# Performance work log

Hardware: AMD Instinct MI355X
Metric: run time of the kernel (lower is better)

## Reference

```python
import jax, jax.numpy as jnp
import numpy as np

EMBED_DIM = 1024
NUM_HEADS = 16
HEAD_DIM = EMBED_DIM // NUM_HEADS
B, T = 4, 2048


def setup_inputs() -> dict:
    key = jax.random.key(0)
    ks = jax.random.split(key, 5)
    s = 1.0 / np.sqrt(EMBED_DIM)
    x = jax.random.normal(ks[0], (B, T, EMBED_DIM), dtype=jnp.float32)
    attention_mask = jnp.ones((B, 1, 1, T), dtype=jnp.int32)
    # torch Linear weights: qkv (3E, E), out (E, E); store transposed for x @ W
    W_qkv = jax.random.uniform(ks[1], (EMBED_DIM, 3 * EMBED_DIM), jnp.float32, -s, s)
    b_qkv = jax.random.uniform(ks[2], (3 * EMBED_DIM,), jnp.float32, -s, s)
    W_out = jax.random.uniform(ks[3], (EMBED_DIM, EMBED_DIM), jnp.float32, -s, s)
    b_out = jax.random.uniform(ks[4], (EMBED_DIM,), jnp.float32, -s, s)
    return {"x": x, "attention_mask": attention_mask,
            "W_qkv": W_qkv, "b_qkv": b_qkv, "W_out": W_out, "b_out": b_out}


def reference(x, attention_mask, W_qkv, b_qkv, W_out, b_out):
    Bq, Tq, E = x.shape
    qkv = x @ W_qkv + b_qkv                              # [B,T,3E]
    qkv = qkv.reshape(Bq, Tq, 3, NUM_HEADS, HEAD_DIM)
    qkv = jnp.transpose(qkv, (2, 0, 3, 1, 4))            # [3,B,H,T,d]
    q, k, v = qkv[0], qkv[1], qkv[2]
    scores = jnp.einsum('bhqd,bhkd->bhqk', q, k) / jnp.sqrt(
        jnp.asarray(HEAD_DIM, x.dtype))                  # [B,H,T,T]
    scores = jnp.where(attention_mask == 0, jnp.asarray(-jnp.inf, x.dtype), scores)
    attn = jax.nn.softmax(scores, axis=-1)
    ctx = jnp.einsum('bhqk,bhkd->bhqd', attn, v)         # [B,H,T,d]
    ctx = jnp.transpose(ctx, (0, 2, 1, 3)).reshape(Bq, Tq, E)
    return ctx @ W_out + b_out
```

## Files before the change

kernel.cpp:

```cpp
#include <hip/hip_runtime.h>
#include <hip/hip_bf16.h>
#include <stdint.h>


typedef __attribute__((ext_vector_type(8))) short short8;
typedef __attribute__((ext_vector_type(4))) float f32x4;
typedef __attribute__((ext_vector_type(16))) float f32x16;
typedef __attribute__((ext_vector_type(4))) unsigned short ushort4_t;
typedef __attribute__((ext_vector_type(8))) unsigned short ushort8_t;

#define SEQ 2048
#define EDIM 1024
#define QSCALE 0.18033688011112042f

__device__ __forceinline__ unsigned short f2bf(float x) {
  union { float f; uint32_t u; } v; v.f = x;
  uint32_t r = v.u + 0x7fffu + ((v.u >> 16) & 1u);
  return (unsigned short)(r >> 16);
}

__device__ __forceinline__ uint32_t cvtpk(float lo, float hi) {
  uint32_t r;
  asm("v_cvt_pk_bf16_f32 %0, %1, %2" : "=v"(r) : "v"(lo), "v"(hi));
  return r;
}

__device__ __forceinline__ float exp2_raw(float x) {
  float r;
  asm("v_exp_f32 %0, %1" : "=v"(r) : "v"(x));
  return r;
}

__device__ __forceinline__ void gload_lds16(const void* g, void* l) {
  typedef __attribute__((address_space(1))) const unsigned int gu32;
  typedef __attribute__((address_space(3))) unsigned int lu32;
  __builtin_amdgcn_global_load_lds((gu32*)g, (lu32*)l, 16, 0, 0);
}

__global__ void k_prep(const float* __restrict__ x,
                       unsigned short* __restrict__ xb,
                       const float* __restrict__ Wq,
                       unsigned short* __restrict__ wqt,
                       const float* __restrict__ Wo,
                       unsigned short* __restrict__ wot) {
  __shared__ float tile[32][33];
  const int id = blockIdx.x;
  if (id < 4096) {
    const int i = id * 256 + threadIdx.x;
    const float4* p = ((const float4*)x) + (size_t)i * 2;
    float4 a = p[0], b = p[1];
    ushort8_t v;
    v[0] = f2bf(a.x); v[1] = f2bf(a.y); v[2] = f2bf(a.z); v[3] = f2bf(a.w);
    v[4] = f2bf(b.x); v[5] = f2bf(b.y); v[6] = f2bf(b.z); v[7] = f2bf(b.w);
    ((ushort8_t*)xb)[i] = v;
    return;
  }
  const float* W;
  unsigned short* Wt;
  int N, bx, by;
  if (id < 7168) { W = Wq; Wt = wqt; N = 3072; bx = (id - 4096) % 96; by = (id - 4096) / 96; }
  else           { W = Wo; Wt = wot; N = 1024; bx = (id - 7168) % 32; by = (id - 7168) / 32; }
  const int K = 1024;
  const int c0 = bx * 32, r0 = by * 32;
  const int tx = threadIdx.x & 31, ty = threadIdx.x >> 5;
#pragma unroll
  for (int i = 0; i < 4; ++i) {
    int r = ty + i * 8;
    tile[r][tx] = W[(size_t)(r0 + r) * N + c0 + tx];
  }
  __syncthreads();
#pragma unroll
  for (int i = 0; i < 4; ++i) {
    int r = ty + i * 8;
    Wt[(size_t)(c0 + r) * K + r0 + tx] = f2bf(tile[tx][r]);
  }
}

template <int EPI, int NBX>
__global__ __launch_bounds__(256, 2) void k_gemm(
    const unsigned short* __restrict__ A, const unsigned short* __restrict__ Bt,
    const float* __restrict__ bias, unsigned short* __restrict__ Qo,
    unsigned short* __restrict__ Ko, unsigned short* __restrict__ VTo,
    float* __restrict__ Out) {
  __shared__ unsigned short As[2][2][128 * 32];
  __shared__ unsigned short Bs[2][2][128 * 32];
  const int tid = threadIdx.x;
  const int lane = tid & 63, wid = tid >> 6;
  const int wr = wid >> 1, wc = wid & 1;
  const int g = lane >> 4, r = lane & 15;
  const int lid = blockIdx.y * NBX + blockIdx.x;
  const int total = NBX * gridDim.y;
  const int id = (lid & 7) * (total >> 3) + (lid >> 3);
  const int m0 = (id / NBX) * 128, n0 = (id % NBX) * 128;

  const int row0 = tid >> 2, sl0 = tid & 3;
  const unsigned short* a0 = A + (size_t)(m0 + row0) * 1024 + sl0 * 8;
  const unsigned short* a1 = A + (size_t)(m0 + 64 + row0) * 1024 + sl0 * 8;
  const unsigned short* b0 = Bt + (size_t)(n0 + row0) * 1024 + sl0 * 8;
  const unsigned short* b1 = Bt + (size_t)(n0 + 64 + row0) * 1024 + sl0 * 8;
  char* adst = (char*)As + wid * 64 * 16;
  char* bdst = (char*)Bs + wid * 64 * 16;

  auto STAGE = [&](int buf) {
    const int bo = buf * 16384;
    gload_lds16(a0,      adst + bo);
    gload_lds16(a1,      adst + bo + 4096);
    gload_lds16(a0 + 32, adst + bo + 8192);
    gload_lds16(a1 + 32, adst + bo + 8192 + 4096);
    gload_lds16(b0,      bdst + bo);
    gload_lds16(b1,      bdst + bo + 4096);
    gload_lds16(b0 + 32, bdst + bo + 8192);
    gload_lds16(b1 + 32, bdst + bo + 8192 + 4096);
    a0 += 64; a1 += 64; b0 += 64; b1 += 64;
  };

  f32x4 zero4 = {0.f, 0.f, 0.f, 0.f};
  f32x4 acc[4][4];
#pragma unroll
  for (int mi = 0; mi < 4; ++mi)
#pragma unroll
    for (int ni = 0; ni < 4; ++ni) acc[mi][ni] = zero4;

  STAGE(0);
  asm volatile("s_waitcnt vmcnt(0)" ::: "memory");
  __builtin_amdgcn_s_barrier();

  for (int t = 0; t < 16; ++t) {
    const int cur = t & 1;
    if (t < 15) STAGE(cur ^ 1);
#pragma unroll
    for (int sub = 0; sub < 2; ++sub) {
      short8 af[4], bf[4];
#pragma unroll
      for (int mi = 0; mi < 4; ++mi)
        af[mi] = *(const short8*)&As[cur][sub][(wr * 64 + mi * 16 + r) * 32 + g * 8];
#pragma unroll
      for (int ni = 0; ni < 4; ++ni)
        bf[ni] = *(const short8*)&Bs[cur][sub][(wc * 64 + ni * 16 + r) * 32 + g * 8];
#pragma unroll
      for (int mi = 0; mi < 4; ++mi)
#pragma unroll
        for (int ni = 0; ni < 4; ++ni)
          acc[mi][ni] = __builtin_amdgcn_mfma_f32_16x16x32_bf16(
              af[mi], bf[ni], acc[mi][ni], 0, 0, 0);
    }
    asm volatile("s_waitcnt vmcnt(0)" ::: "memory");
    __builtin_amdgcn_s_barrier();
  }

#pragma unroll
  for (int mi = 0; mi < 4; ++mi) {
#pragma unroll
    for (int ni = 0; ni < 4; ++ni) {
      const int n = n0 + wc * 64 + ni * 16 + r;
      const float bv = bias[n];
      const int mbase = m0 + wr * 64 + mi * 16 + g * 4;
      if (EPI == 0) {
        const int sec = n >> 10, e = n & 1023, h = e >> 6, dd = e & 63;
        const int b = mbase >> 11, t = mbase & 2047;
        if (sec == 2) {
          ushort4_t pk;
#pragma unroll
          for (int j = 0; j < 4; ++j) pk[j] = f2bf(acc[mi][ni][j] + bv);
          *(ushort4_t*)&VTo[(((size_t)b * 16 + h) * 64 + dd) * 2048 + t] = pk;
        } else {
          unsigned short* dst = (sec == 0) ? Qo : Ko;
          const float scl = (sec == 0) ? QSCALE : 1.0f;
#pragma unroll
          for (int j = 0; j < 4; ++j)
            dst[(((size_t)b * 16 + h) * 2048 + t + j) * 64 + dd] =
                f2bf((acc[mi][ni][j] + bv) * scl);
        }
      } else {
#pragma unroll
        for (int j = 0; j < 4; ++j)
          Out[(size_t)(mbase + j) * 1024 + n] = acc[mi][ni][j] + bv;
      }
    }
  }
}

__global__ __launch_bounds__(512, 4) void k_attn(
    const unsigned short* __restrict__ Qg, const unsigned short* __restrict__ Kg,
    const unsigned short* __restrict__ VTg, const int* __restrict__ maskp,
    unsigned short* __restrict__ ctx) {
  __shared__ unsigned short Ks[2][64 * 64];
  __shared__ unsigned short Vs[2][64 * 64];
  const int tid = threadIdx.x, lane = tid & 63, wid = tid >> 6;
  const int q = lane & 31, hi = lane >> 5;
  const int id = blockIdx.x;
  const int slot = id >> 3;
  const int bh = (id & 7) * 8 + (slot >> 3);
  const int b = bh >> 4, h = bh & 15;
  const int q0 = (slot & 7) * 256 + wid * 32;
  const int qr = q0 + q;

  const unsigned short* Qb = Qg + (size_t)bh * SEQ * 64;
  const unsigned short* Kb = Kg + (size_t)bh * SEQ * 64;
  const unsigned short* Vb = VTg + (size_t)bh * 64 * SEQ;
  const int* mb = maskp + b * SEQ;

  const int r0_ = tid >> 3, sl0_ = (tid & 7) ^ (r0_ & 7);
  const unsigned short* kp0 = Kb + r0_ * 64 + sl0_ * 8;
  const unsigned short* vp0 = Vb + (size_t)r0_ * SEQ + sl0_ * 8;
  char* kbase = (char*)Ks[0] + wid * 1024;
  char* vbase = (char*)Vs[0] + wid * 1024;

  auto STAGE = [&](int buf) {
    const int bo = buf * 8192;
    gload_lds16(kp0, kbase + bo);
    gload_lds16(vp0, vbase + bo);
    kp0 += 64 * 64;
    vp0 += 64;
  };

  short8 qf[4];
#pragma unroll
  for (int ds = 0; ds < 4; ++ds)
    qf[ds] = *(const short8*)&Qb[(size_t)qr * 64 + ds * 16 + hi * 8];

  short8 onesf;
#pragma unroll
  for (int j = 0; j < 8; ++j) onesf[j] = (short)0x3F80;

  f32x16 z16 = {0.f,0.f,0.f,0.f,0.f,0.f,0.f,0.f,0.f,0.f,0.f,0.f,0.f,0.f,0.f,0.f};
  f32x16 o0 = z16, o1 = z16;
  f32x16 osum = z16;
  const int kb4 = hi * 4;

  STAGE(0);
  const int* mptr = mb + lane;
  int mv = mptr[0];
  mptr += 64;

  for (int t = 0; t < 32; ++t) {
    const int cur = t & 1;
    __syncthreads();
    int mvn = 1;
    if (t < 31) {
      STAGE(cur ^ 1);
      mvn = mptr[0];
      mptr += 64;
    }
    const unsigned long long bits = __ballot(mv != 0);
    mv = mvn;

    const char* KsB = (const char*)Ks[cur];
    const char* VsB = (const char*)Vs[cur];
    f32x16 c0 = z16, c1 = z16;
    __builtin_amdgcn_s_setprio(1);
#pragma unroll
    for (int ds = 0; ds < 4; ++ds) {
      const int sl = ds * 2 + hi;
      short8 ka0 = *(const short8*)(KsB + q * 128 + ((sl ^ (q & 7)) * 16));
      short8 ka1 = *(const short8*)(KsB + (32 + q) * 128 + ((sl ^ (q & 7)) * 16));
      c0 = __builtin_amdgcn_mfma_f32_32x32x16_bf16(ka0, qf[ds], c0, 0, 0, 0);
      c1 = __builtin_amdgcn_mfma_f32_32x32x16_bf16(ka1, qf[ds], c1, 0, 0, 0);
    }
    __builtin_amdgcn_s_setprio(0);

#pragma unroll
    for (int i = 0; i < 16; ++i) {
      c0[i] = exp2_raw(c0[i]);
      c1[i] = exp2_raw(c1[i]);
    }
    if (bits != ~0ull) {
#pragma unroll
      for (int i = 0; i < 16; ++i) {
        const int k0 = (i & 3) + 8 * (i >> 2) + kb4;
        if (!((bits >> k0) & 1)) c0[i] = 0.f;
        if (!((bits >> (k0 + 32)) & 1)) c1[i] = 0.f;
      }
    }

    short8 pf[4];
#pragma unroll
    for (int sub = 0; sub < 2; ++sub) {
      uint32_t w[8];
#pragma unroll
      for (int j = 0; j < 8; ++j)
        w[j] = sub ? cvtpk(c1[2 * j], c1[2 * j + 1])
                   : cvtpk(c0[2 * j], c0[2 * j + 1]);
      asm("v_permlane32_swap_b32 %0, %1" : "+v"(w[0]), "+v"(w[2]));
      asm("v_permlane32_swap_b32 %0, %1" : "+v"(w[1]), "+v"(w[3]));
      asm("v_permlane32_swap_b32 %0, %1" : "+v"(w[4]), "+v"(w[6]));
      asm("v_permlane32_swap_b32 %0, %1" : "+v"(w[5]), "+v"(w[7]));
      union { uint32_t u[4]; short8 s; } ua, ub;
      ua.u[0] = w[0]; ua.u[1] = w[1]; ua.u[2] = w[2]; ua.u[3] = w[3];
      ub.u[0] = w[4]; ub.u[1] = w[5]; ub.u[2] = w[6]; ub.u[3] = w[7];
      pf[sub * 2] = ua.s;
      pf[sub * 2 + 1] = ub.s;
    }

    __builtin_amdgcn_s_setprio(1);
#pragma unroll
    for (int ks = 0; ks < 4; ++ks) {
      const int sl = ks * 2 + hi;
      short8 va0 = *(const short8*)(VsB + q * 128 + ((sl ^ (q & 7)) * 16));
      short8 va1 = *(const short8*)(VsB + (32 + q) * 128 + ((sl ^ (q & 7)) * 16));
      o0 = __builtin_amdgcn_mfma_f32_32x32x16_bf16(va0, pf[ks], o0, 0, 0, 0);
      o1 = __builtin_amdgcn_mfma_f32_32x32x16_bf16(va1, pf[ks], o1, 0, 0, 0);
      osum = __builtin_amdgcn_mfma_f32_32x32x16_bf16(onesf, pf[ks], osum,
                                                     0, 0, 0);
    }
    __builtin_amdgcn_s_setprio(0);
  }

  const float inv = 1.f / osum[0];
#pragma unroll
  for (int ns = 0; ns < 2; ++ns) {
#pragma unroll
    for (int g_ = 0; g_ < 4; ++g_) {
      ushort4_t v4;
#pragma unroll
      for (int e = 0; e < 4; ++e) {
        const float val = (ns ? o1[g_ * 4 + e] : o0[g_ * 4 + e]) * inv;
        v4[e] = f2bf(val);
      }
      *(ushort4_t*)&ctx[((size_t)b * SEQ + qr) * 1024 + h * 64 + ns * 32 +
                        g_ * 8 + hi * 4] = v4;
    }
  }
}

extern "C" void kernel_launch(void* const* d_in, const int* in_sizes, int n_in,
                              void* d_out, int out_size, void* d_ws,
                              size_t ws_size, hipStream_t stream) {
  const float* x = (const float*)d_in[0];
  const int* mask = (const int*)d_in[1];
  const float* Wqkv = (const float*)d_in[2];
  const float* bqkv = (const float*)d_in[3];
  const float* Wout = (const float*)d_in[4];
  const float* bout = (const float*)d_in[5];
  float* out = (float*)d_out;

  unsigned short* ws = (unsigned short*)d_ws;
  unsigned short* xb = ws;
  unsigned short* wqt = ws + 8388608;
  unsigned short* wot = ws + 11534336;
  unsigned short* Q = ws + 12582912;
  unsigned short* K = ws + 20971520;
  unsigned short* VT = ws + 29360128;
  unsigned short* ctx = xb;

  k_prep<<<8192, 256, 0, stream>>>(x, xb, Wqkv, wqt, Wout, wot);
  k_gemm<0, 24><<<dim3(24, 64), 256, 0, stream>>>(xb, wqt, bqkv, Q, K, VT,
                                                  nullptr);
  k_attn<<<512, 512, 0, stream>>>(Q, K, VT, mask, ctx);
  k_gemm<1, 8><<<dim3(8, 64), 256, 0, stream>>>(ctx, wot, bout, nullptr,
                                                nullptr, nullptr, out);
}
```

Before: 189.4 us.

## Load K/V fragments directly from global memory instead of staging through LDS

The attention kernel no longer double-buffers K and V tiles in shared memory with async global-to-LDS loads and per-iteration barriers. Each wave now reads its MFMA operand fragments straight from global memory, relying on L2 and L1 caching for reuse across the 8 waves in a block. This removes the __syncthreads and LDS traffic, but each wave issues redundant global loads and the prefetch overlap with compute is lost, so latency is exposed.

```diff
diff --git a/kernel.cpp b/kernel.cpp
--- a/kernel.cpp
+++ b/kernel.cpp
@@ -184,8 +184,6 @@
     const unsigned short* __restrict__ Qg, const unsigned short* __restrict__ Kg,
     const unsigned short* __restrict__ VTg, const int* __restrict__ maskp,
     unsigned short* __restrict__ ctx) {
-  __shared__ unsigned short Ks[2][64 * 64];
-  __shared__ unsigned short Vs[2][64 * 64];
   const int tid = threadIdx.x, lane = tid & 63, wid = tid >> 6;
   const int q = lane & 31, hi = lane >> 5;
   const int id = blockIdx.x;
@@ -200,24 +198,15 @@
   const unsigned short* Vb = VTg + (size_t)bh * 64 * SEQ;
   const int* mb = maskp + b * SEQ;
 
-  const int r0_ = tid >> 3, sl0_ = (tid & 7) ^ (r0_ & 7);
-  const unsigned short* kp0 = Kb + r0_ * 64 + sl0_ * 8;
-  const unsigned short* vp0 = Vb + (size_t)r0_ * SEQ + sl0_ * 8;
-  char* kbase = (char*)Ks[0] + wid * 1024;
-  char* vbase = (char*)Vs[0] + wid * 1024;
-
-  auto STAGE = [&](int buf) {
-    const int bo = buf * 8192;
-    gload_lds16(kp0, kbase + bo);
-    gload_lds16(vp0, vbase + bo);
-    kp0 += 64 * 64;
-    vp0 += 64;
-  };
-
   short8 qf[4];
 #pragma unroll
   for (int ds = 0; ds < 4; ++ds)
     qf[ds] = *(const short8*)&Qb[(size_t)qr * 64 + ds * 16 + hi * 8];
+
+  const unsigned short* kp0 = Kb + q * 64 + hi * 8;
+  const unsigned short* kp1 = Kb + (32 + q) * 64 + hi * 8;
+  const unsigned short* vp0 = Vb + (size_t)q * SEQ + hi * 8;
+  const unsigned short* vp1 = Vb + (size_t)(32 + q) * SEQ + hi * 8;
 
   short8 onesf;
 #pragma unroll
@@ -228,32 +217,15 @@
   f32x16 osum = z16;
   const int kb4 = hi * 4;
 
-  STAGE(0);
-  const int* mptr = mb + lane;
-  int mv = mptr[0];
-  mptr += 64;
-
   for (int t = 0; t < 32; ++t) {
-    const int cur = t & 1;
-    __syncthreads();
-    int mvn = 1;
-    if (t < 31) {
-      STAGE(cur ^ 1);
-      mvn = mptr[0];
-      mptr += 64;
-    }
-    const unsigned long long bits = __ballot(mv != 0);
-    mv = mvn;
-
-    const char* KsB = (const char*)Ks[cur];
-    const char* VsB = (const char*)Vs[cur];
+    const unsigned long long bits = __ballot(mb[t * 64 + lane] != 0);
+
     f32x16 c0 = z16, c1 = z16;
     __builtin_amdgcn_s_setprio(1);
 #pragma unroll
     for (int ds = 0; ds < 4; ++ds) {
-      const int sl = ds * 2 + hi;
-      short8 ka0 = *(const short8*)(KsB + q * 128 + ((sl ^ (q & 7)) * 16));
-      short8 ka1 = *(const short8*)(KsB + (32 + q) * 128 + ((sl ^ (q & 7)) * 16));
+      short8 ka0 = *(const short8*)(kp0 + ds * 16);
+      short8 ka1 = *(const short8*)(kp1 + ds * 16);
       c0 = __builtin_amdgcn_mfma_f32_32x32x16_bf16(ka0, qf[ds], c0, 0, 0, 0);
       c1 = __builtin_amdgcn_mfma_f32_32x32x16_bf16(ka1, qf[ds], c1, 0, 0, 0);
     }
@@ -295,15 +267,17 @@
     __builtin_amdgcn_s_setprio(1);
 #pragma unroll
     for (int ks = 0; ks < 4; ++ks) {
-      const int sl = ks * 2 + hi;
-      short8 va0 = *(const short8*)(VsB + q * 128 + ((sl ^ (q & 7)) * 16));
-      short8 va1 = *(const short8*)(VsB + (32 + q) * 128 + ((sl ^ (q & 7)) * 16));
+      short8 va0 = *(const short8*)(vp0 + ks * 16);
+      short8 va1 = *(const short8*)(vp1 + ks * 16);
       o0 = __builtin_amdgcn_mfma_f32_32x32x16_bf16(va0, pf[ks], o0, 0, 0, 0);
       o1 = __builtin_amdgcn_mfma_f32_32x32x16_bf16(va1, pf[ks], o1, 0, 0, 0);
       osum = __builtin_amdgcn_mfma_f32_32x32x16_bf16(onesf, pf[ks], osum,
                                                      0, 0, 0);
     }
     __builtin_amdgcn_s_setprio(0);
+
+    kp0 += 64 * 64; kp1 += 64 * 64;
+    vp0 += 64; vp1 += 64;
   }
 
   const float inv = 1.f / osum[0];
```

Result: slower. 341.9 us (+80.5%).

## Store GEMM and attention LDS tiles in MFMA fragment order for linear reads

Applied to the files above, without the earlier changes.

Reorganizes the shared-memory layout in both the projection GEMM and attention kernels so that global-to-LDS loads scatter data directly into per-lane MFMA fragment order. Each lane then reads its operand with a single contiguous lane*16 offset. This removes the XOR swizzle and row/column address arithmetic and avoids bank conflicts on ds_read. The cost is less coalesced global loads, since each lane now fetches 16-byte chunks from scattered rows.

```diff
diff --git a/kernel.cpp b/kernel.cpp
--- a/kernel.cpp
+++ b/kernel.cpp
@@ -82,8 +82,8 @@
     const float* __restrict__ bias, unsigned short* __restrict__ Qo,
     unsigned short* __restrict__ Ko, unsigned short* __restrict__ VTo,
     float* __restrict__ Out) {
-  __shared__ unsigned short As[2][2][128 * 32];
-  __shared__ unsigned short Bs[2][2][128 * 32];
+  __shared__ unsigned short As[2 * 8192];
+  __shared__ unsigned short Bs[2 * 8192];
   const int tid = threadIdx.x;
   const int lane = tid & 63, wid = tid >> 6;
   const int wr = wid >> 1, wc = wid & 1;
@@ -93,25 +93,29 @@
   const int id = (lid & 7) * (total >> 3) + (lid >> 3);
   const int m0 = (id / NBX) * 128, n0 = (id % NBX) * 128;
 
-  const int row0 = tid >> 2, sl0 = tid & 3;
-  const unsigned short* a0 = A + (size_t)(m0 + row0) * 1024 + sl0 * 8;
-  const unsigned short* a1 = A + (size_t)(m0 + 64 + row0) * 1024 + sl0 * 8;
-  const unsigned short* b0 = Bt + (size_t)(n0 + row0) * 1024 + sl0 * 8;
-  const unsigned short* b1 = Bt + (size_t)(n0 + 64 + row0) * 1024 + sl0 * 8;
-  char* adst = (char*)As + wid * 64 * 16;
-  char* bdst = (char*)Bs + wid * 64 * 16;
+  const unsigned short* ap[4];
+  const unsigned short* bp[4];
+#pragma unroll
+  for (int i = 0; i < 4; ++i) {
+    const int slot = i * 256 + tid;
+    const int sub = slot >> 9, mi = (slot >> 7) & 3, wrr = (slot >> 6) & 1;
+    const int l = slot & 63;
+    const int row = wrr * 64 + mi * 16 + (l & 15);
+    const int dof = sub * 32 + (l >> 4) * 8;
+    ap[i] = A + (size_t)(m0 + row) * 1024 + dof;
+    bp[i] = Bt + (size_t)(n0 + row) * 1024 + dof;
+  }
+  char* adst = (char*)As + wid * 1024;
+  char* bdst = (char*)Bs + wid * 1024;
 
   auto STAGE = [&](int buf) {
     const int bo = buf * 16384;
-    gload_lds16(a0,      adst + bo);
-    gload_lds16(a1,      adst + bo + 4096);
-    gload_lds16(a0 + 32, adst + bo + 8192);
-    gload_lds16(a1 + 32, adst + bo + 8192 + 4096);
-    gload_lds16(b0,      bdst + bo);
-    gload_lds16(b1,      bdst + bo + 4096);
-    gload_lds16(b0 + 32, bdst + bo + 8192);
-    gload_lds16(b1 + 32, bdst + bo + 8192 + 4096);
-    a0 += 64; a1 += 64; b0 += 64; b1 += 64;
+#pragma unroll
+    for (int i = 0; i < 4; ++i) {
+      gload_lds16(ap[i], adst + bo + i * 4096);
+      gload_lds16(bp[i], bdst + bo + i * 4096);
+      ap[i] += 64; bp[i] += 64;
+    }
   };
 
   f32x4 zero4 = {0.f, 0.f, 0.f, 0.f};
@@ -120,6 +124,10 @@
   for (int mi = 0; mi < 4; ++mi)
 #pragma unroll
     for (int ni = 0; ni < 4; ++ni) acc[mi][ni] = zero4;
+
+  const int myoff = lane * 16;
+  const char* abase = (const char*)As + wr * 1024 + myoff;
+  const char* bbase = (const char*)Bs + wc * 1024 + myoff;
 
   STAGE(0);
   asm volatile("s_waitcnt vmcnt(0)" ::: "memory");
@@ -128,15 +136,16 @@
   for (int t = 0; t < 16; ++t) {
     const int cur = t & 1;
     if (t < 15) STAGE(cur ^ 1);
+    const int co = cur * 16384;
 #pragma unroll
     for (int sub = 0; sub < 2; ++sub) {
       short8 af[4], bf[4];
 #pragma unroll
       for (int mi = 0; mi < 4; ++mi)
-        af[mi] = *(const short8*)&As[cur][sub][(wr * 64 + mi * 16 + r) * 32 + g * 8];
+        af[mi] = *(const short8*)(abase + co + sub * 8192 + mi * 2048);
 #pragma unroll
       for (int ni = 0; ni < 4; ++ni)
-        bf[ni] = *(const short8*)&Bs[cur][sub][(wc * 64 + ni * 16 + r) * 32 + g * 8];
+        bf[ni] = *(const short8*)(bbase + co + sub * 8192 + ni * 2048);
 #pragma unroll
       for (int mi = 0; mi < 4; ++mi)
 #pragma unroll
@@ -184,8 +193,8 @@
     const unsigned short* __restrict__ Qg, const unsigned short* __restrict__ Kg,
     const unsigned short* __restrict__ VTg, const int* __restrict__ maskp,
     unsigned short* __restrict__ ctx) {
-  __shared__ unsigned short Ks[2][64 * 64];
-  __shared__ unsigned short Vs[2][64 * 64];
+  __shared__ unsigned short Ks[2 * 4096];
+  __shared__ unsigned short Vs[2 * 4096];
   const int tid = threadIdx.x, lane = tid & 63, wid = tid >> 6;
   const int q = lane & 31, hi = lane >> 5;
   const int id = blockIdx.x;
@@ -200,11 +209,13 @@
   const unsigned short* Vb = VTg + (size_t)bh * 64 * SEQ;
   const int* mb = maskp + b * SEQ;
 
-  const int r0_ = tid >> 3, sl0_ = (tid & 7) ^ (r0_ & 7);
-  const unsigned short* kp0 = Kb + r0_ * 64 + sl0_ * 8;
-  const unsigned short* vp0 = Vb + (size_t)r0_ * SEQ + sl0_ * 8;
-  char* kbase = (char*)Ks[0] + wid * 1024;
-  char* vbase = (char*)Vs[0] + wid * 1024;
+  const int sds = tid >> 7, shalf = (tid >> 6) & 1, sl_ = tid & 63;
+  const int srow = shalf * 32 + (sl_ & 31);
+  const int schnk = (sds * 2 + (sl_ >> 5)) * 8;
+  const unsigned short* kp0 = Kb + srow * 64 + schnk;
+  const unsigned short* vp0 = Vb + (size_t)srow * SEQ + schnk;
+  char* kbase = (char*)Ks + wid * 1024;
+  char* vbase = (char*)Vs + wid * 1024;
 
   auto STAGE = [&](int buf) {
     const int bo = buf * 8192;
@@ -227,6 +238,7 @@
   f32x16 o0 = z16, o1 = z16;
   f32x16 osum = z16;
   const int kb4 = hi * 4;
+  const int myoff = lane * 16;
 
   STAGE(0);
   const int* mptr = mb + lane;
@@ -245,15 +257,14 @@
     const unsigned long long bits = __ballot(mv != 0);
     mv = mvn;
 
-    const char* KsB = (const char*)Ks[cur];
-    const char* VsB = (const char*)Vs[cur];
+    const char* KsB = (const char*)Ks + cur * 8192 + myoff;
+    const char* VsB = (const char*)Vs + cur * 8192 + myoff;
     f32x16 c0 = z16, c1 = z16;
     __builtin_amdgcn_s_setprio(1);
 #pragma unroll
     for (int ds = 0; ds < 4; ++ds) {
-      const int sl = ds * 2 + hi;
-      short8 ka0 = *(const short8*)(KsB + q * 128 + ((sl ^ (q & 7)) * 16));
-      short8 ka1 = *(const short8*)(KsB + (32 + q) * 128 + ((sl ^ (q & 7)) * 16));
+      short8 ka0 = *(const short8*)(KsB + ds * 2048);
+      short8 ka1 = *(const short8*)(KsB + ds * 2048 + 1024);
       c0 = __builtin_amdgcn_mfma_f32_32x32x16_bf16(ka0, qf[ds], c0, 0, 0, 0);
       c1 = __builtin_amdgcn_mfma_f32_32x32x16_bf16(ka1, qf[ds], c1, 0, 0, 0);
     }
@@ -295,9 +306,8 @@
     __builtin_amdgcn_s_setprio(1);
 #pragma unroll
     for (int ks = 0; ks < 4; ++ks) {
-      const int sl = ks * 2 + hi;
-      short8 va0 = *(const short8*)(VsB + q * 128 + ((sl ^ (q & 7)) * 16));
-      short8 va1 = *(const short8*)(VsB + (32 + q) * 128 + ((sl ^ (q & 7)) * 16));
+      short8 va0 = *(const short8*)(VsB + ks * 2048);
+      short8 va1 = *(const short8*)(VsB + ks * 2048 + 1024);
       o0 = __builtin_amdgcn_mfma_f32_32x32x16_bf16(va0, pf[ks], o0, 0, 0, 0);
       o1 = __builtin_amdgcn_mfma_f32_32x32x16_bf16(va1, pf[ks], o1, 0, 0, 0);
       osum = __builtin_amdgcn_mfma_f32_32x32x16_bf16(onesf, pf[ks], osum,
```

Result: slower. 248.9 us (+31.4%).
